# Kernel tuning notes

Measured on AMD Instinct MI355X. Metric: run time of the kernel, lower is better.

## Reference

```python
import jax, jax.numpy as jnp
import numpy as np

N = 50000; E = 800000; IN_DIM = 128; HID = 128; OUT = 128; K_TARGET = 5000


def setup_inputs() -> dict:
    key = jax.random.key(0)
    ks = jax.random.split(key, 7)
    x = jax.random.normal(ks[0], (N, IN_DIM), jnp.float32)
    edge_index = jax.random.randint(ks[1], (2, E), 0, N, dtype=jnp.int32)
    W1 = jax.random.normal(ks[2], (IN_DIM, HID), jnp.float32) / np.float32(np.sqrt(IN_DIM))
    b1 = jnp.zeros((HID,), jnp.float32)
    W2 = jax.random.normal(ks[3], (HID, OUT), jnp.float32) / np.float32(np.sqrt(HID))
    b2 = jnp.zeros((OUT,), jnp.float32)
    w_score = jax.random.normal(ks[4], (HID,), jnp.float32) / np.float32(np.sqrt(HID))
    W_skip = jax.random.normal(ks[5], (HID, OUT), jnp.float32) / np.float32(np.sqrt(HID))
    b_skip = jnp.zeros((OUT,), jnp.float32)
    return dict(x=x, edge_index=edge_index, W1=W1, b1=b1, W2=W2, b2=b2,
                w_score=w_score, W_skip=W_skip, b_skip=b_skip)


def _gcn(h_in, row, col, W, b, nseg, edge_w=None):
    # PyG GCNConv with add_self_loops=True, normalize=True:
    # deg[i] = sum of incoming edge weights at col + 1 (self loop, weight 1)
    h = h_in @ W
    w = edge_w if edge_w is not None else jnp.ones(row.shape, h.dtype)
    deg = jax.ops.segment_sum(w, col, num_segments=nseg) + 1.0
    dinv = jax.lax.rsqrt(deg)
    norm = dinv[row] * w * dinv[col]                     # [E]
    agg = jax.ops.segment_sum(norm[:, None] * h[row], col, num_segments=nseg)
    agg = agg + (dinv * dinv)[:, None] * h               # self-loop messages
    return agg + b


def _forward(x, edge_index, W1, b1, W2, b2, w_score, W_skip, b_skip):
    row, col = edge_index[0], edge_index[1]
    n = x.shape[0]
    e = row.shape[0]
    x1 = jax.nn.relu(_gcn(x, row, col, W1, b1, n))       # conv1 + relu (dropout: eval mode)
    raw = x1 @ w_score                                    # [N]
    x1g = x1 * jnp.tanh(raw)[:, None]                     # gated features
    K = min(K_TARGET, n)
    _, kept = jax.lax.top_k(raw, K)                       # sorted desc, ties -> lower index
    keep_mask = jnp.zeros((n,), bool).at[kept].set(True)
    deg = jax.ops.segment_sum(jnp.ones((e,), jnp.int32), row, num_segments=n)  # bincount(row)
    # neighbor insertion order: edge i appends col[i] to neigh[row[i]] (order 2i),
    # then row[i] to neigh[col[i]] (order 2i+1)
    owners = jnp.concatenate([row, col])
    neighs = jnp.concatenate([col, row])
    e_ar = jnp.arange(e, dtype=jnp.int32)
    order = jnp.concatenate([2 * e_ar, 2 * e_ar + 1])
    M = 2 * e + 2
    valid = keep_mask[neighs]
    comp = deg[neighs] * M + (M - 1 - order)
    comp = jnp.where(valid, comp, -1)
    best = jax.ops.segment_max(comp, owners, num_segments=n)
    has_valid = best >= 0
    is_best = valid & (comp == best[owners])              # unique per owner (order unique)
    best_neigh = jax.ops.segment_max(jnp.where(is_best, neighs, -1), owners, num_segments=n)
    cluster_of = jnp.full((n,), -1, jnp.int32).at[kept].set(jnp.arange(K, dtype=jnp.int32))
    best_global_kept = kept[jnp.argmax(deg[kept])]
    fallback = cluster_of[best_global_kept]
    assigned = jnp.where(has_valid, cluster_of[jnp.maximum(best_neigh, 0)], fallback)
    cluster_id = jnp.where(keep_mask, cluster_of, assigned)
    # mean pool per cluster (Kc == K since kept nodes carry ids 0..K-1)
    sums = jax.ops.segment_sum(x1g, cluster_id, num_segments=K)
    counts = jnp.maximum(jax.ops.segment_sum(jnp.ones((n,), x.dtype), cluster_id, num_segments=K), 1.0)
    x_p = sums / counts[:, None]
    # coarse edges: duplicates summed == unique edges weighted by counts; self-pairs dropped
    cu, cv = cluster_id[row], cluster_id[col]
    w_e = (cu != cv).astype(x.dtype)
    x_p = _gcn(x_p, cu, cv, W2, b2, K, edge_w=w_e)        # conv2 with edge_weight
    logits = x_p[cluster_id] + x1 @ W_skip + b_skip       # broadcast up + skip
    return logits


def reference(x, edge_index, W1, b1, W2, b2, w_score, W_skip, b_skip):
    logits = _forward(x, edge_index, W1, b1, W2, b2, w_score, W_skip, b_skip)
    return (logits, 0.0)
```

## Files before the change

kernel.cpp:

```cpp
#include <hip/hip_runtime.h>
#include <cstdint>

#define N_NODES 50000
#define N_EDGES 800000
#define DIM 128
#define KSEL 5000
#define MCONST (2 * N_EDGES + 2)
#define PCH 64
#define PCH2 16
#define CANDCAP 8192
#define TM 4
#define KRB ((KSEL + 255) / 256)
#define GPERS 2048

typedef unsigned long long u64;
typedef uint32_t u32;

#define FMA4(A_, S_, W_) { (A_).x = fmaf((S_), (W_).x, (A_).x); (A_).y = fmaf((S_), (W_).y, (A_).y); \
                           (A_).z = fmaf((S_), (W_).z, (A_).z); (A_).w = fmaf((S_), (W_).w, (A_).w); }

__device__ __forceinline__ void gemm_tile_body(const float4* __restrict__ W4,
                                               float xs[32][DIM], float4 acc[TM],
                                               int tx, int ty) {
#pragma unroll 8
  for (int k4 = 0; k4 < 32; k4++) {
    float4 xv[TM];
#pragma unroll
    for (int m = 0; m < TM; m++) xv[m] = *(const float4*)&xs[ty + 8 * m][k4 * 4];
#pragma unroll
    for (int j = 0; j < 4; j++) {
      float4 wv = W4[(k4 * 4 + j) * 32 + tx];
#pragma unroll
      for (int m = 0; m < TM; m++) {
        float sv = (j == 0) ? xv[m].x : (j == 1) ? xv[m].y : (j == 2) ? xv[m].z : xv[m].w;
        FMA4(acc[m], sv, wv);
      }
    }
  }
}

__global__ void gemm_tiled(const float* __restrict__ X, const float* __restrict__ W,
                           float* __restrict__ Y, int nrows) {
  __shared__ float xs[32][DIM];
  int tx = threadIdx.x & 31, ty = threadIdx.x >> 5;
  int rbase = blockIdx.x * 32;
  int nval = min(32, nrows - rbase);
  const float4* X4 = (const float4*)(X + (size_t)rbase * DIM);
  float4* xs4 = (float4*)&xs[0][0];
  for (int i = threadIdx.x; i < 32 * 32; i += 256)
    if ((i >> 5) < nval) xs4[i] = X4[i];
  __syncthreads();
  float4 acc[TM];
#pragma unroll
  for (int m = 0; m < TM; m++) acc[m] = make_float4(0.f, 0.f, 0.f, 0.f);
  gemm_tile_body((const float4*)W, xs, acc, tx, ty);
#pragma unroll
  for (int m = 0; m < TM; m++) {
    int r = rbase + ty + 8 * m;
    if (r < nrows) ((float4*)(Y + (size_t)r * DIM))[tx] = acc[m];
  }
}

__global__ void gemm_tiled_div(const float* __restrict__ S, const int* __restrict__ counts,
                               const float* __restrict__ W, float* __restrict__ Y, int nrows) {
  __shared__ float xs[32][DIM];
  int tx = threadIdx.x & 31, ty = threadIdx.x >> 5;
  int rbase = blockIdx.x * 32;
  int nval = min(32, nrows - rbase);
  const float4* X4 = (const float4*)(S + (size_t)rbase * DIM);
  float4* xs4 = (float4*)&xs[0][0];
  for (int i = threadIdx.x; i < 32 * 32; i += 256) {
    int rr = i >> 5;
    if (rr < nval) {
      float inv = 1.0f / (float)max(counts[rbase + rr], 1);
      float4 v = X4[i];
      v.x *= inv; v.y *= inv; v.z *= inv; v.w *= inv;
      xs4[i] = v;
    }
  }
  __syncthreads();
  float4 acc[TM];
#pragma unroll
  for (int m = 0; m < TM; m++) acc[m] = make_float4(0.f, 0.f, 0.f, 0.f);
  gemm_tile_body((const float4*)W, xs, acc, tx, ty);
#pragma unroll
  for (int m = 0; m < TM; m++) {
    int r = rbase + ty + 8 * m;
    if (r < nrows) ((float4*)(Y + (size_t)r * DIM))[tx] = acc[m];
  }
}

__global__ void final_tiled(const float* __restrict__ x1, const float* __restrict__ Wsk,
                            const float* __restrict__ bsk, const float* __restrict__ xp2,
                            const int* __restrict__ cluster, float* __restrict__ out) {
  __shared__ float xs[32][DIM];
  int tx = threadIdx.x & 31, ty = threadIdx.x >> 5;
  int rbase = blockIdx.x * 32;
  int nval = min(32, N_NODES - rbase);
  const float4* X4 = (const float4*)(x1 + (size_t)rbase * DIM);
  float4* xs4 = (float4*)&xs[0][0];
  for (int i = threadIdx.x; i < 32 * 32; i += 256)
    if ((i >> 5) < nval) xs4[i] = X4[i];
  __syncthreads();
  float4 acc[TM];
#pragma unroll
  for (int m = 0; m < TM; m++) acc[m] = make_float4(0.f, 0.f, 0.f, 0.f);
  gemm_tile_body((const float4*)Wsk, xs, acc, tx, ty);
  float4 bv = ((const float4*)bsk)[tx];
#pragma unroll
  for (int m = 0; m < TM; m++) {
    int r = rbase + ty + 8 * m;
    if (r < N_NODES) {
      int cl = cluster[r];
      cl = (cl < 0) ? 0 : (cl >= KSEL ? KSEL - 1 : cl);
      float4 pv = ((const float4*)(xp2 + (size_t)cl * DIM))[tx];
      float4 o;
      o.x = acc[m].x + bv.x + pv.x;
      o.y = acc[m].y + bv.y + pv.y;
      o.z = acc[m].z + bv.z + pv.z;
      o.w = acc[m].w + bv.w + pv.w;
      ((float4*)(out + (size_t)r * DIM))[tx] = o;
    }
  }
  if (blockIdx.x == 0 && threadIdx.x == 0) out[(size_t)N_NODES * DIM] = 0.0f;
}

__global__ void deg_kernel(const int* __restrict__ row, const int* __restrict__ col,
                           int* deg1, int* deg2) {
  int e = blockIdx.x * blockDim.x + threadIdx.x;
  if (e < N_EDGES) {
    atomicAdd(&deg1[col[e]], 1);
    atomicAdd(&deg2[row[e]], 1);
  }
}

__global__ void rsqrt_kernel(const int* __restrict__ deg, float* __restrict__ dinv, int n) {
  int i = blockIdx.x * blockDim.x + threadIdx.x;
  if (i < n) dinv[i] = rsqrtf((float)deg[i] + 1.0f);
}

__global__ void scan_local(const int* __restrict__ in, int* __restrict__ out,
                           int* __restrict__ bsum, int n) {
  __shared__ int s[256];
  int i = blockIdx.x * 256 + threadIdx.x;
  int v = (i < n) ? in[i] : 0;
  s[threadIdx.x] = v;
  __syncthreads();
  for (int off = 1; off < 256; off <<= 1) {
    int t = (threadIdx.x >= off) ? s[threadIdx.x - off] : 0;
    __syncthreads();
    s[threadIdx.x] += t;
    __syncthreads();
  }
  if (i < n) out[i] = s[threadIdx.x] - v;
  if (threadIdx.x == 255) bsum[blockIdx.x] = s[255];
}

__global__ void scan_bsum(int* bsum, int nb) {
  __shared__ int s[256];
  int v = (threadIdx.x < nb) ? bsum[threadIdx.x] : 0;
  s[threadIdx.x] = v;
  __syncthreads();
  for (int off = 1; off < 256; off <<= 1) {
    int t = (threadIdx.x >= off) ? s[threadIdx.x - off] : 0;
    __syncthreads();
    s[threadIdx.x] += t;
    __syncthreads();
  }
  if (threadIdx.x < nb) bsum[threadIdx.x] = s[threadIdx.x] - v;
}

__global__ void scan_add(int* out, const int* __restrict__ bsum, int n) {
  int i = blockIdx.x * 256 + threadIdx.x;
  if (i < n) out[i] += bsum[blockIdx.x];
}

__global__ void scan_small(const int* __restrict__ in, int* __restrict__ out, int n) {
  __shared__ int s[256];
  __shared__ int carry;
  if (threadIdx.x == 0) carry = 0;
  __syncthreads();
  for (int base = 0; base < n; base += 256) {
    int i = base + threadIdx.x;
    int v = (i < n) ? in[i] : 0;
    s[threadIdx.x] = v;
    __syncthreads();
    for (int off = 1; off < 256; off <<= 1) {
      int t = (threadIdx.x >= off) ? s[threadIdx.x - off] : 0;
      __syncthreads();
      s[threadIdx.x] += t;
      __syncthreads();
    }
    int c = carry;
    if (i < n) out[i] = c + s[threadIdx.x] - v;
    __syncthreads();
    if (threadIdx.x == 255) carry = c + s[255];
    __syncthreads();
  }
  if (threadIdx.x == 0) out[n] = carry;
}

__global__ void fill_ecsr(const int* __restrict__ row, const int* __restrict__ col,
                          const int* __restrict__ start, int* cursor, int* payload) {
  int e = blockIdx.x * blockDim.x + threadIdx.x;
  if (e < N_EDGES) {
    int c = col[e];
    int p = start[c] + atomicAdd(&cursor[c], 1);
    if (p >= 0 && p < N_EDGES) payload[p] = row[e];
  }
}

__global__ void fill_members(const int* __restrict__ cluster, const int* __restrict__ startn,
                             int* cursorn, int* members) {
  int i = blockIdx.x * blockDim.x + threadIdx.x;
  if (i < N_NODES) {
    int c = cluster[i];
    int p = startn[c] + atomicAdd(&cursorn[c], 1);
    if (p >= 0 && p < N_NODES) members[p] = i;
  }
}

__global__ void gcn1_gather(const int* __restrict__ srcs, const int* __restrict__ start,
                            const int* __restrict__ deg1, const float* __restrict__ dinv,
                            const float* __restrict__ h, const float* __restrict__ b1,
                            const float* __restrict__ wscore,
                            float* __restrict__ B, float* __restrict__ gate,
                            u64* __restrict__ key) {
  int lane = threadIdx.x & 63;
  int g = lane >> 5, l32 = lane & 31;
  int gbase = g << 5;
  int wid = blockIdx.x * (blockDim.x >> 6) + (threadIdx.x >> 6);
  int nw = gridDim.x * (blockDim.x >> 6);
  const float4* h4 = (const float4*)h;
  float4 wsv = ((const float4*)wscore)[l32];
  float4 b1v = ((const float4*)b1)[l32];
  for (int v = wid; v < N_NODES; v += nw) {
    int s0 = start[v], n = deg1[v];
    float di = dinv[v];
    float4 hself = h4[(size_t)v * 32 + l32];
    float4 acc0 = make_float4(0.f, 0.f, 0.f, 0.f);
    float4 acc1 = make_float4(0.f, 0.f, 0.f, 0.f);
    for (int base = 0; base < n; base += 64) {
      int mm = min(64, n - base);
      int idx = base + (l32 << 1) + g;
      int csv = (idx < n) ? srcs[s0 + idx] : 0;
      float wvl = (idx < n) ? dinv[csv] : 0.f;
      int cnt = (mm + 1 - g) >> 1;
      int i = 0;
      for (; i + 3 < cnt; i += 4) {
        int r0 = __shfl(csv, gbase + i),     r1 = __shfl(csv, gbase + i + 1);
        int r2 = __shfl(csv, gbase + i + 2), r3 = __shfl(csv, gbase + i + 3);
        float w0 = __shfl(wvl, gbase + i),     w1 = __shfl(wvl, gbase + i + 1);
        float w2 = __shfl(wvl, gbase + i + 2), w3 = __shfl(wvl, gbase + i + 3);
        float4 a0 = h4[(size_t)r0 * 32 + l32];
        float4 a1 = h4[(size_t)r1 * 32 + l32];
        float4 a2 = h4[(size_t)r2 * 32 + l32];
        float4 a3 = h4[(size_t)r3 * 32 + l32];
        FMA4(acc0, w0, a0); FMA4(acc1, w1, a1);
        FMA4(acc0, w2, a2); FMA4(acc1, w3, a3);
      }
      for (; i + 1 < cnt; i += 2) {
        int r0 = __shfl(csv, gbase + i), r1 = __shfl(csv, gbase + i + 1);
        float w0 = __shfl(wvl, gbase + i), w1 = __shfl(wvl, gbase + i + 1);
        float4 a0 = h4[(size_t)r0 * 32 + l32];
        float4 a1 = h4[(size_t)r1 * 32 + l32];
        FMA4(acc0, w0, a0); FMA4(acc1, w1, a1);
      }
      if (i < cnt) {
        int r0 = __shfl(csv, gbase + i);
        float w0 = __shfl(wvl, gbase + i);
        float4 a0 = h4[(size_t)r0 * 32 + l32];
        FMA4(acc0, w0, a0);
      }
    }
    acc0.x += acc1.x; acc0.y += acc1.y; acc0.z += acc1.z; acc0.w += acc1.w;
    acc0.x += __shfl_xor(acc0.x, 32);
    acc0.y += __shfl_xor(acc0.y, 32);
    acc0.z += __shfl_xor(acc0.z, 32);
    acc0.w += __shfl_xor(acc0.w, 32);
    float dd = di * di;
    float4 vv;
    vv.x = acc0.x * di + dd * hself.x + b1v.x;
    vv.y = acc0.y * di + dd * hself.y + b1v.y;
    vv.z = acc0.z * di + dd * hself.z + b1v.z;
    vv.w = acc0.w * di + dd * hself.w + b1v.w;
    vv.x = vv.x > 0.f ? vv.x : 0.f;
    vv.y = vv.y > 0.f ? vv.y : 0.f;
    vv.z = vv.z > 0.f ? vv.z : 0.f;
    vv.w = vv.w > 0.f ? vv.w : 0.f;
    if (lane < 32) ((float4*)(B + (size_t)v * DIM))[l32] = vv;
    float sd = vv.x * wsv.x + vv.y * wsv.y + vv.z * wsv.z + vv.w * wsv.w;
    sd += __shfl_xor(sd, 1);
    sd += __shfl_xor(sd, 2);
    sd += __shfl_xor(sd, 4);
    sd += __shfl_xor(sd, 8);
    sd += __shfl_xor(sd, 16);
    if (lane == 0) {
      gate[v] = tanhf(sd);
      u32 b = __float_as_uint(sd);
      if ((b << 1) == 0u) b = 0u;
      u32 ord = (b & 0x80000000u) ? ~b : (b | 0x80000000u);
      key[v] = (((u64)(~ord)) << 32) | (u32)v;
    }
  }
}

__global__ void hist1_kernel(const u64* __restrict__ key, int* __restrict__ hist) {
  int i = blockIdx.x * blockDim.x + threadIdx.x;
  if (i < N_NODES) atomicAdd(&hist[(int)(key[i] >> 52)], 1);
}

__global__ void hist2_kernel(const u64* __restrict__ key, const int* __restrict__ selb,
                             int* __restrict__ hist) {
  int i = blockIdx.x * blockDim.x + threadIdx.x;
  if (i < N_NODES) {
    u64 k = key[i];
    if ((int)(k >> 52) == selb[0]) atomicAdd(&hist[(int)((k >> 40) & 0xFFF)], 1);
  }
}

__global__ void pick_kernel(const int* __restrict__ hist, int K_imm, int* __restrict__ selb,
                            int rem_in_slot, int bin_out_slot, int rem_out_slot) {
  __shared__ int s[256];
  int t = threadIdx.x;
  int base = t * 16;
  int loc[16];
  int sum = 0;
#pragma unroll
  for (int k = 0; k < 16; k++) { loc[k] = hist[base + k]; sum += loc[k]; }
  s[t] = sum;
  __syncthreads();
  for (int off = 1; off < 256; off <<= 1) {
    int v = (t >= off) ? s[t - off] : 0;
    __syncthreads();
    s[t] += v;
    __syncthreads();
  }
  int target = (K_imm >= 0) ? K_imm : selb[rem_in_slot];
  int prev = (t == 0) ? 0 : s[t - 1];
  if (prev < target && target <= s[t]) {
    int cum = prev;
#pragma unroll
    for (int k = 0; k < 16; k++) {
      cum += loc[k];
      if (cum >= target) {
        selb[bin_out_slot] = base + k;
        selb[rem_out_slot] = target - (cum - loc[k]);
        break;
      }
    }
  }
}

__global__ void collect_kernel(const u64* __restrict__ key, const int* __restrict__ selb,
                               u64* __restrict__ cand, int* __restrict__ ccnt) {
  int i = blockIdx.x * blockDim.x + threadIdx.x;
  if (i < N_NODES) {
    u64 k = key[i];
    if ((int)(k >> 52) == selb[0] && (int)((k >> 40) & 0xFFF) == selb[2]) {
      int p = atomicAdd(ccnt, 1);
      if (p < CANDCAP) cand[p] = k;
    }
  }
}

__global__ void thresh_kernel(const u64* __restrict__ cand, const int* __restrict__ ccnt,
                              const int* __restrict__ selb, u64* __restrict__ T) {
  int c = min(*ccnt, CANDCAP);
  int R = selb[3];
  for (int p = threadIdx.x; p < c; p += 256) {
    u64 kp = cand[p];
    int cnt = 0;
    for (int q = 0; q < c; q++) cnt += (cand[q] < kp) ? 1 : 0;
    if (cnt == R - 1) *T = kp;
  }
}

__global__ void compact_kernel(const u64* __restrict__ key, const u64* __restrict__ T,
                               int* __restrict__ krank, u64* __restrict__ kkey,
                               int* __restrict__ kidx, int* __restrict__ kcnt) {
  int i = blockIdx.x * blockDim.x + threadIdx.x;
  if (i < N_NODES) {
    krank[i] = -1;
    u64 k = key[i];
    if (k <= *T) {
      int p = atomicAdd(kcnt, 1);
      if (p < KSEL + 16) {
        kkey[p] = k;
        kidx[p] = i;
      }
    }
  }
}

__global__ void krank_count(const u64* __restrict__ kkey, int* __restrict__ rankc) {
  int p = blockIdx.x * 256 + threadIdx.x;
  u64 mykey = (p < KSEL) ? kkey[p] : ~0ull;
  int qbase = blockIdx.y * 256;
  __shared__ u64 sk[256];
  int j = qbase + threadIdx.x;
  sk[threadIdx.x] = (j < KSEL) ? kkey[j] : ~0ull;
  __syncthreads();
  int lim = min(256, KSEL - qbase);
  int cnt = 0;
#pragma unroll 8
  for (int q = 0; q < lim; q++) cnt += (sk[q] < mykey) ? 1 : 0;
  if (p < KSEL && cnt) atomicAdd(&rankc[p], cnt);
}

__global__ void krank_final(const int* __restrict__ rankc, const int* __restrict__ kidx,
                            const int* __restrict__ deg2, int* __restrict__ krank,
                            u64* fbkey) {
  int p = blockIdx.x * 256 + threadIdx.x;
  if (p < KSEL) {
    int node = kidx[p];
    if (node >= 0 && node < N_NODES) {
      int cnt = rankc[p];
      krank[node] = cnt;
      u64 fk = (((u64)(deg2[node] + 1)) << 32) | (u32)(KSEL - 1 - cnt);
      atomicMax(fbkey, fk);
    }
  }
}

__global__ void bestneigh_kernel(const int* __restrict__ row, const int* __restrict__ col,
                                 const int* __restrict__ krank, const int* __restrict__ deg2,
                                 u64* __restrict__ best) {
  int e = blockIdx.x * blockDim.x + threadIdx.x;
  if (e < N_EDGES) {
    int r = row[e], c = col[e];
    if (krank[c] >= 0) {
      u64 comp = (u64)deg2[c] * (u64)MCONST + (u64)(MCONST - 1 - 2 * e);
      atomicMax(&best[r], comp + 1);
    }
    if (krank[r] >= 0) {
      u64 comp = (u64)deg2[r] * (u64)MCONST + (u64)(MCONST - 2 - 2 * e);
      atomicMax(&best[c], comp + 1);
    }
  }
}

__global__ void assign_kernel(const int* __restrict__ krank, const u64* __restrict__ best,
                              const int* __restrict__ row, const int* __restrict__ col,
                              const u64* __restrict__ fbkey,
                              int* __restrict__ cluster, int* __restrict__ counts) {
  int i = blockIdx.x * blockDim.x + threadIdx.x;
  if (i >= N_NODES) return;
  int c;
  int rk = krank[i];
  if (rk >= 0) {
    c = rk;
  } else {
    u64 b = best[i];
    if (b > 0) {
      u64 comp = b - 1;
      int rem = (int)(comp % (u64)MCONST);
      int ord = MCONST - 1 - rem;
      int e = ord >> 1;
      int nb = (ord & 1) ? row[e] : col[e];
      c = krank[nb];
    } else {
      c = KSEL - 1 - (int)((*fbkey) & 0xffffffffu);
    }
  }
  c = (c < 0) ? 0 : (c >= KSEL ? KSEL - 1 : c);
  cluster[i] = c;
  atomicAdd(&counts[c], 1);
}

__global__ void pool_chunk(const int* __restrict__ members, const int* __restrict__ startn,
                           const int* __restrict__ cluster,
                           const float* __restrict__ x1, const float* __restrict__ gate,
                           float* __restrict__ sums) {
  int cb = blockIdx.x * PCH;
  if (cb >= N_NODES) return;
  int ce = min(cb + PCH, N_NODES);
  __shared__ int pl[PCH];
  for (int k = threadIdx.x; k < ce - cb; k += DIM) pl[k] = members[cb + k];
  __syncthreads();
  int c = cluster[pl[0]];
  int segend = startn[c + 1];
  int t = threadIdx.x;
  float acc = 0.f;
  for (int k = cb; k < ce; k++) {
    int j = pl[k - cb];
    acc = fmaf(gate[j], x1[j * DIM + t], acc);
    int k1 = k + 1;
    if (k1 == segend || k1 == ce) {
      atomicAdd(&sums[c * DIM + t], acc);
      acc = 0.f;
      if (k1 == segend && k1 < ce) {
        while (c < KSEL - 1 && startn[c + 1] <= k1) c++;
        segend = startn[c + 1];
      }
    }
  }
}

__global__ void map_csrc(const int* __restrict__ payload, const int* __restrict__ cluster,
                         int* __restrict__ csrc) {
  int p = blockIdx.x * blockDim.x + threadIdx.x;
  if (p < N_EDGES) csrc[p] = cluster[payload[p]];
}

__global__ void cdeg_kernel(const int* __restrict__ csrc, const int* __restrict__ start,
                            const int* __restrict__ deg1, const int* __restrict__ cluster,
                            int* __restrict__ degc) {
  int v = blockIdx.x * blockDim.x + threadIdx.x;
  if (v >= N_NODES) return;
  int cv = cluster[v];
  int s0 = start[v], n = deg1[v], cnt = 0;
  for (int k = 0; k < n; k++) cnt += (csrc[s0 + k] != cv) ? 1 : 0;
  if (cnt) atomicAdd(&degc[cv], cnt);
}

__global__ void coarse_chunk(const int* __restrict__ members, const int* __restrict__ startn,
                             const int* __restrict__ cluster,
                             const int* __restrict__ start, const int* __restrict__ deg1,
                             const int* __restrict__ csrc, const float* __restrict__ dinvc,
                             const float* __restrict__ h2, float* __restrict__ agg2) {
  int cb = blockIdx.x * PCH2;
  if (cb >= N_NODES) return;
  int ce = min(cb + PCH2, N_NODES);
  int t = threadIdx.x;
  int g = t >> 5, l32 = t & 31;
  int gbase = (g & 1) << 5;
  __shared__ int pm[PCH2];
  __shared__ float red4[4][DIM];
  for (int k = t; k < ce - cb; k += 128) pm[k] = members[cb + k];
  __syncthreads();
  int c = cluster[pm[0]];
  int segend = startn[c + 1];
  const float4* h24 = (const float4*)h2;
  float4 acc = make_float4(0.f, 0.f, 0.f, 0.f);
  int m = cb;
  int v0 = pm[0];
  int s0 = start[v0], n = deg1[v0];
  while (m < ce) {
    int m1 = m + 1;
    int s0n = 0, nn = 0;
    if (m1 < ce) { int v1 = pm[m1 - cb]; s0n = start[v1]; nn = deg1[v1]; }
    for (int base = 0; base < n; base += 128) {
      int mm = min(128, n - base);
      int idx = base + (l32 << 2) + g;
      int csv = (idx < n) ? csrc[s0 + idx] : 0;
      float wvl = (idx < n && csv != c) ? dinvc[csv] : 0.f;
      int cnt = (mm + 3 - g) >> 2;
      int i = 0;
      for (; i + 3 < cnt; i += 4) {
        int r0 = __shfl(csv, gbase + i),     r1 = __shfl(csv, gbase + i + 1);
        int r2 = __shfl(csv, gbase + i + 2), r3 = __shfl(csv, gbase + i + 3);
        float w0 = __shfl(wvl, gbase + i),     w1 = __shfl(wvl, gbase + i + 1);
        float w2 = __shfl(wvl, gbase + i + 2), w3 = __shfl(wvl, gbase + i + 3);
        float4 a0 = h24[(size_t)r0 * 32 + l32];
        float4 a1 = h24[(size_t)r1 * 32 + l32];
        float4 a2 = h24[(size_t)r2 * 32 + l32];
        float4 a3 = h24[(size_t)r3 * 32 + l32];
        FMA4(acc, w0, a0); FMA4(acc, w1, a1);
        FMA4(acc, w2, a2); FMA4(acc, w3, a3);
      }
      for (; i < cnt; i++) {
        int r0 = __shfl(csv, gbase + i);
        float w0 = __shfl(wvl, gbase + i);
        float4 a0 = h24[(size_t)r0 * 32 + l32];
        FMA4(acc, w0, a0);
      }
    }
    if (m1 == segend || m1 == ce) {
      *(float4*)&red4[g][l32 * 4] = acc;
      __syncthreads();
      float sv = red4[0][t] + red4[1][t] + red4[2][t] + red4[3][t];
      atomicAdd(&agg2[(size_t)c * DIM + t], sv);
      __syncthreads();
      acc = make_float4(0.f, 0.f, 0.f, 0.f);
      if (m1 == segend && m1 < ce) {
        while (c < KSEL - 1 && startn[c + 1] <= m1) c++;
        segend = startn[c + 1];
      }
    }
    m = m1; s0 = s0n; n = nn;
  }
}

__global__ void combine2(const float* __restrict__ agg2, const float* __restrict__ h2,
                         const float* __restrict__ dinvc, const float* __restrict__ b2,
                         float* __restrict__ xp2) {
  int gid = blockIdx.x * blockDim.x + threadIdx.x;
  int c = gid >> 7, d = gid & 127;
  if (c < KSEL) {
    float dc = dinvc[c];
    xp2[gid] = agg2[gid] * dc + dc * dc * h2[gid] + b2[d];
  }
}

extern "C" void kernel_launch(void* const* d_in, const int* in_sizes, int n_in,
                              void* d_out, int out_size, void* d_ws, size_t ws_size,
                              hipStream_t stream) {
  const float* x      = (const float*)d_in[0];
  const int*   eidx   = (const int*)d_in[1];
  const float* W1     = (const float*)d_in[2];
  const float* b1     = (const float*)d_in[3];
  const float* W2     = (const float*)d_in[4];
  const float* b2     = (const float*)d_in[5];
  const float* wscore = (const float*)d_in[6];
  const float* Wsk    = (const float*)d_in[7];
  const float* bsk    = (const float*)d_in[8];
  float* out = (float*)d_out;

  const int* row = eidx;
  const int* col = eidx + N_EDGES;

  char* ws = (char*)d_ws;
#define ALIGN16(v) (((v) + 15) & ~(size_t)15)
  size_t off = 0;
#define CARVE(ptr_t, name, bytes) ptr_t name = (ptr_t)(ws + off); off = ALIGN16(off + (bytes))
  size_t h_off = off;
  CARVE(float*, h, (size_t)N_NODES * DIM * 4);
  CARVE(float*, B, (size_t)N_NODES * DIM * 4);
  CARVE(int*, payload, (size_t)N_EDGES * 4);
  CARVE(u64*, key, (size_t)N_NODES * 8);
  CARVE(float*, gate, (size_t)N_NODES * 4);
  CARVE(float*, dinv, (size_t)N_NODES * 4);
  CARVE(int*, start, (size_t)N_NODES * 4);
  CARVE(int*, bsum, 256 * 4);
  size_t zA = off;
  CARVE(int*, deg1, (size_t)N_NODES * 4);
  CARVE(int*, deg2, (size_t)N_NODES * 4);
  CARVE(int*, cursor, (size_t)N_NODES * 4);
  size_t zAsize = off - zA;

  size_t ho = h_off;
#define CARVE2(ptr_t, name, bytes) ptr_t name = (ptr_t)(ws + ho); ho = ALIGN16(ho + (bytes))
  CARVE2(int*, cluster, (size_t)N_NODES * 4);
  CARVE2(int*, members, (size_t)N_NODES * 4);
  CARVE2(int*, startn, (size_t)(KSEL + 1) * 4);
  CARVE2(float*, dinvc, (size_t)KSEL * 4);
  CARVE2(float*, h2, (size_t)KSEL * DIM * 4);
  CARVE2(int*, csrc, (size_t)N_EDGES * 4);
  size_t zB = ho;
  CARVE2(u64*, best, (size_t)N_NODES * 8);
  CARVE2(int*, counts, (size_t)KSEL * 4);
  CARVE2(int*, degc, (size_t)KSEL * 4);
  CARVE2(int*, cursorn, (size_t)KSEL * 4);
  CARVE2(float*, sums, (size_t)KSEL * DIM * 4);
  CARVE2(float*, agg2, (size_t)KSEL * DIM * 4);
  CARVE2(u64*, fbkey, 8);
  CARVE2(int*, hist1, 4096 * 4);
  CARVE2(int*, hist2, 4096 * 4);
  CARVE2(int*, rankc, (size_t)KSEL * 4);
  CARVE2(int*, ccnt, 16);
  CARVE2(int*, kcnt, 16);
  size_t zBsize = ho - zB;
  CARVE2(int*, krank, (size_t)N_NODES * 4);
  CARVE2(u64*, cand, (size_t)CANDCAP * 8);
  CARVE2(u64*, kkey, (size_t)(KSEL + 16) * 8);
  CARVE2(int*, kidx, (size_t)(KSEL + 16) * 4);
  CARVE2(int*, selb, 4 * 4);
  CARVE2(u64*, Tkey, 8);
  float* xp2 = sums;
  (void)ws_size; (void)out_size; (void)n_in; (void)in_sizes;

  const int eb  = (N_EDGES + 255) / 256;
  const int nb  = (N_NODES + 255) / 256;
  const int kbs = (KSEL + 255) / 256;
  const int pcb = (N_NODES + PCH - 1) / PCH;
  const int ccb = (N_NODES + PCH2 - 1) / PCH2;
  const int gtb = (N_NODES + 31) / 32;
  const int gkb = (KSEL + 31) / 32;

  hipMemsetAsync(ws + zA, 0, zAsize, stream);

  gemm_tiled<<<gtb, 256, 0, stream>>>(x, W1, h, N_NODES);
  deg_kernel<<<eb, 256, 0, stream>>>(row, col, deg1, deg2);
  rsqrt_kernel<<<nb, 256, 0, stream>>>(deg1, dinv, N_NODES);
  scan_local<<<nb, 256, 0, stream>>>(deg1, start, bsum, N_NODES);
  scan_bsum<<<1, 256, 0, stream>>>(bsum, nb);
  scan_add<<<nb, 256, 0, stream>>>(start, bsum, N_NODES);
  fill_ecsr<<<eb, 256, 0, stream>>>(row, col, start, cursor, payload);
  gcn1_gather<<<GPERS, 256, 0, stream>>>(payload, start, deg1, dinv, h, b1, wscore,
                                         B, gate, key);
  hipMemsetAsync(ws + zB, 0, zBsize, stream);

  hist1_kernel<<<nb, 256, 0, stream>>>(key, hist1);
  pick_kernel<<<1, 256, 0, stream>>>(hist1, KSEL, selb, 0, 0, 1);
  hist2_kernel<<<nb, 256, 0, stream>>>(key, selb, hist2);
  pick_kernel<<<1, 256, 0, stream>>>(hist2, -1, selb, 1, 2, 3);
  collect_kernel<<<nb, 256, 0, stream>>>(key, selb, cand, ccnt);
  thresh_kernel<<<1, 256, 0, stream>>>(cand, ccnt, selb, Tkey);
  compact_kernel<<<nb, 256, 0, stream>>>(key, Tkey, krank, kkey, kidx, kcnt);
  krank_count<<<dim3(KRB, KRB), 256, 0, stream>>>(kkey, rankc);
  krank_final<<<kbs, 256, 0, stream>>>(rankc, kidx, deg2, krank, fbkey);

  bestneigh_kernel<<<eb, 256, 0, stream>>>(row, col, krank, deg2, best);
  assign_kernel<<<nb, 256, 0, stream>>>(krank, best, row, col, fbkey, cluster, counts);

  scan_small<<<1, 256, 0, stream>>>(counts, startn, KSEL);
  fill_members<<<nb, 256, 0, stream>>>(cluster, startn, cursorn, members);
  pool_chunk<<<pcb, DIM, 0, stream>>>(members, startn, cluster, B, gate, sums);
  map_csrc<<<eb, 256, 0, stream>>>(payload, cluster, csrc);
  cdeg_kernel<<<nb, 256, 0, stream>>>(csrc, start, deg1, cluster, degc);
  rsqrt_kernel<<<kbs, 256, 0, stream>>>(degc, dinvc, KSEL);

  gemm_tiled_div<<<gkb, 256, 0, stream>>>(sums, counts, W2, h2, KSEL);
  coarse_chunk<<<ccb, 128, 0, stream>>>(members, startn, cluster, start, deg1, csrc,
                                        dinvc, h2, agg2);
  combine2<<<(KSEL * DIM) / 256, 256, 0, stream>>>(agg2, h2, dinvc, b2, xp2);

  final_tiled<<<gtb, 256, 0, stream>>>(B, Wsk, bsk, xp2, cluster, out);
}
```

Before: 662.4 us.

## Software-pipeline neighbor index loads in gather kernels and fuse rsqrt into scan

Both gather kernels (gcn1_gather and coarse_chunk) now prefetch the next node's CSR start, degree and first chunk of neighbor indices, plus their dinv weights, while the current node is being aggregated. This hides the dependent-load latency at each node boundary. The coarse kernel also moves the self-cluster exclusion from load time to a per-edge select. Separately, the rsqrt computation is folded into scan_local, removing one kernel launch. In exchange the gather kernels hold more registers, which may lower occupancy.

```diff
diff --git a/kernel.cpp b/kernel.cpp
--- a/kernel.cpp
+++ b/kernel.cpp
@@ -140,10 +140,11 @@
 }
 
 __global__ void scan_local(const int* __restrict__ in, int* __restrict__ out,
-                           int* __restrict__ bsum, int n) {
+                           int* __restrict__ bsum, float* __restrict__ dinv, int n) {
   __shared__ int s[256];
   int i = blockIdx.x * 256 + threadIdx.x;
   int v = (i < n) ? in[i] : 0;
+  if (i < n) dinv[i] = rsqrtf((float)v + 1.0f);
   s[threadIdx.x] = v;
   __syncthreads();
   for (int off = 1; off < 256; off <<= 1) {
@@ -219,6 +220,19 @@
     if (p >= 0 && p < N_NODES) members[p] = i;
   }
 }
+
+#define GBURST4(csv_, wvl_, A0_, A1_) \
+  for (; i + 3 < cnt; i += 4) { \
+    int r0 = __shfl(csv_, gbase + i),     r1 = __shfl(csv_, gbase + i + 1); \
+    int r2 = __shfl(csv_, gbase + i + 2), r3 = __shfl(csv_, gbase + i + 3); \
+    float w0 = __shfl(wvl_, gbase + i),     w1 = __shfl(wvl_, gbase + i + 1); \
+    float w2 = __shfl(wvl_, gbase + i + 2), w3 = __shfl(wvl_, gbase + i + 3); \
+    float4 a0 = hb[(size_t)r0 * 32 + l32]; \
+    float4 a1 = hb[(size_t)r1 * 32 + l32]; \
+    float4 a2 = hb[(size_t)r2 * 32 + l32]; \
+    float4 a3 = hb[(size_t)r3 * 32 + l32]; \
+    FMA4(A0_, w0, a0); FMA4(A1_, w1, a1); \
+    FMA4(A0_, w2, a2); FMA4(A1_, w3, a3); }
 
 __global__ void gcn1_gather(const int* __restrict__ srcs, const int* __restrict__ start,
                             const int* __restrict__ deg1, const float* __restrict__ dinv,
@@ -231,59 +245,82 @@
   int gbase = g << 5;
   int wid = blockIdx.x * (blockDim.x >> 6) + (threadIdx.x >> 6);
   int nw = gridDim.x * (blockDim.x >> 6);
-  const float4* h4 = (const float4*)h;
+  const float4* hb = (const float4*)h;
   float4 wsv = ((const float4*)wscore)[l32];
   float4 b1v = ((const float4*)b1)[l32];
-  for (int v = wid; v < N_NODES; v += nw) {
-    int s0 = start[v], n = deg1[v];
-    float di = dinv[v];
-    float4 hself = h4[(size_t)v * 32 + l32];
+  int idxs = (l32 << 1) + g;
+  int v = wid;
+  if (v >= N_NODES) return;
+  int s0a = start[v], na = deg1[v];
+  float dia = dinv[v];
+  int csvA = (idxs < na) ? srcs[s0a + idxs] : 0;
+  float wvlA = (idxs < na) ? dinv[csvA] : 0.f;
+  int vn = v + nw;
+  int s0b = 0, nb = 0; float dib = 0.f;
+  if (vn < N_NODES) { s0b = start[vn]; nb = deg1[vn]; dib = dinv[vn]; }
+  while (v < N_NODES) {
+    int vq = v + 2 * nw;
+    int s0c = 0, nc = 0; float dic = 0.f;
+    if (vq < N_NODES) { s0c = start[vq]; nc = deg1[vq]; dic = dinv[vq]; }
+    int csvB = 0;
+    if (vn < N_NODES && idxs < nb) csvB = srcs[s0b + idxs];
+    float4 hself = hb[(size_t)v * 32 + l32];
     float4 acc0 = make_float4(0.f, 0.f, 0.f, 0.f);
     float4 acc1 = make_float4(0.f, 0.f, 0.f, 0.f);
-    for (int base = 0; base < n; base += 64) {
-      int mm = min(64, n - base);
-      int idx = base + (l32 << 1) + g;
-      int csv = (idx < n) ? srcs[s0 + idx] : 0;
-      float wvl = (idx < n) ? dinv[csv] : 0.f;
+    {
+      int mm = min(64, na);
       int cnt = (mm + 1 - g) >> 1;
       int i = 0;
-      for (; i + 3 < cnt; i += 4) {
-        int r0 = __shfl(csv, gbase + i),     r1 = __shfl(csv, gbase + i + 1);
-        int r2 = __shfl(csv, gbase + i + 2), r3 = __shfl(csv, gbase + i + 3);
-        float w0 = __shfl(wvl, gbase + i),     w1 = __shfl(wvl, gbase + i + 1);
-        float w2 = __shfl(wvl, gbase + i + 2), w3 = __shfl(wvl, gbase + i + 3);
-        float4 a0 = h4[(size_t)r0 * 32 + l32];
-        float4 a1 = h4[(size_t)r1 * 32 + l32];
-        float4 a2 = h4[(size_t)r2 * 32 + l32];
-        float4 a3 = h4[(size_t)r3 * 32 + l32];
+      GBURST4(csvA, wvlA, acc0, acc1)
+      for (; i + 1 < cnt; i += 2) {
+        int r0 = __shfl(csvA, gbase + i), r1 = __shfl(csvA, gbase + i + 1);
+        float w0 = __shfl(wvlA, gbase + i), w1 = __shfl(wvlA, gbase + i + 1);
+        float4 a0 = hb[(size_t)r0 * 32 + l32];
+        float4 a1 = hb[(size_t)r1 * 32 + l32];
         FMA4(acc0, w0, a0); FMA4(acc1, w1, a1);
-        FMA4(acc0, w2, a2); FMA4(acc1, w3, a3);
-      }
+      }
+      if (i < cnt) {
+        int r0 = __shfl(csvA, gbase + i);
+        float w0 = __shfl(wvlA, gbase + i);
+        float4 a0 = hb[(size_t)r0 * 32 + l32];
+        FMA4(acc0, w0, a0);
+      }
+    }
+    for (int base = 64; base < na; base += 64) {
+      int mm = min(64, na - base);
+      int idx = base + idxs;
+      int csv = (idx < na) ? srcs[s0a + idx] : 0;
+      float wvl = (idx < na) ? dinv[csv] : 0.f;
+      int cnt = (mm + 1 - g) >> 1;
+      int i = 0;
+      GBURST4(csv, wvl, acc0, acc1)
       for (; i + 1 < cnt; i += 2) {
         int r0 = __shfl(csv, gbase + i), r1 = __shfl(csv, gbase + i + 1);
         float w0 = __shfl(wvl, gbase + i), w1 = __shfl(wvl, gbase + i + 1);
-        float4 a0 = h4[(size_t)r0 * 32 + l32];
-        float4 a1 = h4[(size_t)r1 * 32 + l32];
+        float4 a0 = hb[(size_t)r0 * 32 + l32];
+        float4 a1 = hb[(size_t)r1 * 32 + l32];
         FMA4(acc0, w0, a0); FMA4(acc1, w1, a1);
       }
       if (i < cnt) {
         int r0 = __shfl(csv, gbase + i);
         float w0 = __shfl(wvl, gbase + i);
-        float4 a0 = h4[(size_t)r0 * 32 + l32];
+        float4 a0 = hb[(size_t)r0 * 32 + l32];
         FMA4(acc0, w0, a0);
       }
     }
+    float wvlB = 0.f;
+    if (vn < N_NODES && idxs < nb) wvlB = dinv[csvB];
     acc0.x += acc1.x; acc0.y += acc1.y; acc0.z += acc1.z; acc0.w += acc1.w;
     acc0.x += __shfl_xor(acc0.x, 32);
     acc0.y += __shfl_xor(acc0.y, 32);
     acc0.z += __shfl_xor(acc0.z, 32);
     acc0.w += __shfl_xor(acc0.w, 32);
-    float dd = di * di;
+    float dd = dia * dia;
     float4 vv;
-    vv.x = acc0.x * di + dd * hself.x + b1v.x;
-    vv.y = acc0.y * di + dd * hself.y + b1v.y;
-    vv.z = acc0.z * di + dd * hself.z + b1v.z;
-    vv.w = acc0.w * di + dd * hself.w + b1v.w;
+    vv.x = acc0.x * dia + dd * hself.x + b1v.x;
+    vv.y = acc0.y * dia + dd * hself.y + b1v.y;
+    vv.z = acc0.z * dia + dd * hself.z + b1v.z;
+    vv.w = acc0.w * dia + dd * hself.w + b1v.w;
     vv.x = vv.x > 0.f ? vv.x : 0.f;
     vv.y = vv.y > 0.f ? vv.y : 0.f;
     vv.z = vv.z > 0.f ? vv.z : 0.f;
@@ -302,6 +339,8 @@
       u32 ord = (b & 0x80000000u) ? ~b : (b | 0x80000000u);
       key[v] = (((u64)(~ord)) << 32) | (u32)v;
     }
+    v = vn; s0a = s0b; na = nb; dia = dib; csvA = csvB; wvlA = wvlB;
+    vn = vq; s0b = s0c; nb = nc; dib = dic;
   }
 }
 
@@ -514,6 +553,21 @@
   if (cnt) atomicAdd(&degc[cv], cnt);
 }
 
+#define CBURST4(csv_, wvl_) \
+  for (; i + 3 < cnt; i += 4) { \
+    int r0 = __shfl(csv_, gbase + i),     r1 = __shfl(csv_, gbase + i + 1); \
+    int r2 = __shfl(csv_, gbase + i + 2), r3 = __shfl(csv_, gbase + i + 3); \
+    float w0 = __shfl(wvl_, gbase + i),     w1 = __shfl(wvl_, gbase + i + 1); \
+    float w2 = __shfl(wvl_, gbase + i + 2), w3 = __shfl(wvl_, gbase + i + 3); \
+    w0 = (r0 == c) ? 0.f : w0; w1 = (r1 == c) ? 0.f : w1; \
+    w2 = (r2 == c) ? 0.f : w2; w3 = (r3 == c) ? 0.f : w3; \
+    float4 a0 = h24[(size_t)r0 * 32 + l32]; \
+    float4 a1 = h24[(size_t)r1 * 32 + l32]; \
+    float4 a2 = h24[(size_t)r2 * 32 + l32]; \
+    float4 a3 = h24[(size_t)r3 * 32 + l32]; \
+    FMA4(acc, w0, a0); FMA4(acc, w1, a1); \
+    FMA4(acc, w2, a2); FMA4(acc, w3, a3); }
+
 __global__ void coarse_chunk(const int* __restrict__ members, const int* __restrict__ startn,
                              const int* __restrict__ cluster,
                              const int* __restrict__ start, const int* __restrict__ deg1,
@@ -532,40 +586,51 @@
   int c = cluster[pm[0]];
   int segend = startn[c + 1];
   const float4* h24 = (const float4*)h2;
+  int idxs = (l32 << 2) + g;
   float4 acc = make_float4(0.f, 0.f, 0.f, 0.f);
   int m = cb;
   int v0 = pm[0];
-  int s0 = start[v0], n = deg1[v0];
+  int s0a = start[v0], na = deg1[v0];
+  int csvA = (idxs < na) ? csrc[s0a + idxs] : 0;
+  float wvlA = dinvc[csvA];
+  int s0b = 0, nb = 0;
+  if (m + 1 < ce) { int v1 = pm[1]; s0b = start[v1]; nb = deg1[v1]; }
   while (m < ce) {
     int m1 = m + 1;
-    int s0n = 0, nn = 0;
-    if (m1 < ce) { int v1 = pm[m1 - cb]; s0n = start[v1]; nn = deg1[v1]; }
-    for (int base = 0; base < n; base += 128) {
-      int mm = min(128, n - base);
-      int idx = base + (l32 << 2) + g;
-      int csv = (idx < n) ? csrc[s0 + idx] : 0;
-      float wvl = (idx < n && csv != c) ? dinvc[csv] : 0.f;
+    int s0c = 0, nc = 0;
+    if (m + 2 < ce) { int v2 = pm[m + 2 - cb]; s0c = start[v2]; nc = deg1[v2]; }
+    int csvB = 0;
+    if (m1 < ce && idxs < nb) csvB = csrc[s0b + idxs];
+    {
+      int mm = min(128, na);
       int cnt = (mm + 3 - g) >> 2;
       int i = 0;
-      for (; i + 3 < cnt; i += 4) {
-        int r0 = __shfl(csv, gbase + i),     r1 = __shfl(csv, gbase + i + 1);
-        int r2 = __shfl(csv, gbase + i + 2), r3 = __shfl(csv, gbase + i + 3);
-        float w0 = __shfl(wvl, gbase + i),     w1 = __shfl(wvl, gbase + i + 1);
-        float w2 = __shfl(wvl, gbase + i + 2), w3 = __shfl(wvl, gbase + i + 3);
+      CBURST4(csvA, wvlA)
+      for (; i < cnt; i++) {
+        int r0 = __shfl(csvA, gbase + i);
+        float w0 = __shfl(wvlA, gbase + i);
+        w0 = (r0 == c) ? 0.f : w0;
         float4 a0 = h24[(size_t)r0 * 32 + l32];
-        float4 a1 = h24[(size_t)r1 * 32 + l32];
-        float4 a2 = h24[(size_t)r2 * 32 + l32];
-        float4 a3 = h24[(size_t)r3 * 32 + l32];
-        FMA4(acc, w0, a0); FMA4(acc, w1, a1);
-        FMA4(acc, w2, a2); FMA4(acc, w3, a3);
-      }
+        FMA4(acc, w0, a0);
+      }
+    }
+    for (int base = 128; base < na; base += 128) {
+      int mm = min(128, na - base);
+      int idx = base + idxs;
+      int csv = (idx < na) ? csrc[s0a + idx] : 0;
+      float wvl = dinvc[csv];
+      int cnt = (mm + 3 - g) >> 2;
+      int i = 0;
+      CBURST4(csv, wvl)
       for (; i < cnt; i++) {
         int r0 = __shfl(csv, gbase + i);
         float w0 = __shfl(wvl, gbase + i);
+        w0 = (r0 == c) ? 0.f : w0;
         float4 a0 = h24[(size_t)r0 * 32 + l32];
         FMA4(acc, w0, a0);
       }
     }
+    float wvlB = dinvc[csvB];
     if (m1 == segend || m1 == ce) {
       *(float4*)&red4[g][l32 * 4] = acc;
       __syncthreads();
@@ -578,7 +643,8 @@
         segend = startn[c + 1];
       }
     }
-    m = m1; s0 = s0n; n = nn;
+    m = m1; s0a = s0b; na = nb; csvA = csvB; wvlA = wvlB;
+    s0b = s0c; nb = nc;
   }
 }
 
@@ -672,8 +738,7 @@
 
   gemm_tiled<<<gtb, 256, 0, stream>>>(x, W1, h, N_NODES);
   deg_kernel<<<eb, 256, 0, stream>>>(row, col, deg1, deg2);
-  rsqrt_kernel<<<nb, 256, 0, stream>>>(deg1, dinv, N_NODES);
-  scan_local<<<nb, 256, 0, stream>>>(deg1, start, bsum, N_NODES);
+  scan_local<<<nb, 256, 0, stream>>>(deg1, start, bsum, dinv, N_NODES);
   scan_bsum<<<1, 256, 0, stream>>>(bsum, nb);
   scan_add<<<nb, 256, 0, stream>>>(start, bsum, N_NODES);
   fill_ecsr<<<eb, 256, 0, stream>>>(row, col, start, cursor, payload);
```

New measurement: 644.8 us. -2.7%, faster.
